# Kernel optimization log

Measured on AMD Instinct MI355X. Metric: run time of the kernel, lower is better.

## Reference

```python
import jax, jax.numpy as jnp
import numpy as np

HIDDEN = 768
HEADS = 12
HEAD_DIM = HIDDEN // HEADS
BETA = 0.5
BANDWIDTH = 1.0
D_INTRINSIC = 3
LN_EPS = 1e-12


def setup_inputs() -> dict:
    key = jax.random.key(0)
    ks = jax.random.split(key, 10)
    B, S, E = 2, 2048, HIDDEN
    sc = 1.0 / np.sqrt(E)
    return {
        "hidden_states": jax.random.normal(ks[0], (B, S, E), jnp.float32),
        "attention_mask": jnp.zeros((B, S), jnp.float32),
        "Wq": jax.random.normal(ks[1], (E, E), jnp.float32) * sc,
        "bq": jax.random.normal(ks[2], (E,), jnp.float32) * 0.02,
        "Wv": jax.random.normal(ks[3], (E, E), jnp.float32) * sc,
        "bv": jax.random.normal(ks[4], (E,), jnp.float32) * 0.02,
        "Wo": jax.random.normal(ks[5], (E, E), jnp.float32) * sc,
        "bo": jax.random.normal(ks[6], (E,), jnp.float32) * 0.02,
        "ln_g": jnp.ones((E,), jnp.float32),
        "ln_b": jnp.zeros((E,), jnp.float32),
    }


def _layernorm(x, g, b, eps=LN_EPS):
    mu = jnp.mean(x, axis=-1, keepdims=True)
    var = jnp.mean((x - mu) ** 2, axis=-1, keepdims=True)
    return (x - mu) * jax.lax.rsqrt(var + eps) * g + b


def reference(hidden_states, attention_mask, Wq, bq, Wv, bv, Wo, bo, ln_g, ln_b):
    B, S, E = hidden_states.shape
    H, D = HEADS, HEAD_DIM
    # projections (torch Linear: x @ W.T + b)
    q = (hidden_states @ Wq.T + bq).reshape(B, S, H, D).transpose(0, 2, 1, 3)  # [B,H,S,D]
    v = (hidden_states @ Wv.T + bv).reshape(B, S, H, D).transpose(0, 2, 1, 3)  # [B,H,S,D]
    # pairwise Euclidean distance (cdist) via norm expansion, safe sqrt
    qn = jnp.sum(q * q, axis=-1)  # [B,H,S]
    d2 = qn[:, :, :, None] + qn[:, :, None, :] - 2.0 * jnp.einsum("bhid,bhjd->bhij", q, q)
    dist = jnp.sqrt(jnp.maximum(d2, 1e-12))  # [B,H,S,S]
    # mask: positions with attention_mask < 0 get distance 2
    keep = (attention_mask >= 0)  # [B,S]
    pair_keep = keep[:, None, :, None] & keep[:, None, None, :]  # [B,1,S,S]
    dist = jnp.where(pair_keep, dist, 2.0)
    # power-law score + softmax
    attn_score = (1.0 + dist / (BANDWIDTH ** 0.5)) ** (-D_INTRINSIC - BETA)
    attn = jax.nn.softmax(attn_score, axis=-1)
    out = jnp.einsum("bhij,bhjd->bhid", attn, v)  # [B,H,S,D]
    out = out.transpose(0, 2, 1, 3).reshape(B, S, E)
    # ModelSelfOutput: dense + residual + LayerNorm (dropout=0, eval)
    out = out @ Wo.T + bo
    return _layernorm(out + hidden_states, ln_g, ln_b)
```

## Files before the change

kernel.cpp:

```cpp
#include <hip/hip_runtime.h>
#include <hip/hip_bf16.h>
#include <cstdint>
#include <cstddef>

#define S_LEN 2048
#define NH 12
#define HD 64
#define EDIM 768

typedef short bf16x8 __attribute__((ext_vector_type(8)));
typedef float f32x4  __attribute__((ext_vector_type(4)));

__device__ __forceinline__ unsigned short f2bf(float f) {
    return __bfloat16_as_ushort(__float2bfloat16(f));
}
__device__ __forceinline__ float bf2f(unsigned short u) {
    union { unsigned int i; float f; } x;
    x.i = ((unsigned int)u) << 16;
    return x.f;
}
__device__ __forceinline__ float rsq_f32(float x) {
#if __has_builtin(__builtin_amdgcn_rsqf)
    return __builtin_amdgcn_rsqf(x);
#else
    return __builtin_amdgcn_rcpf(__builtin_amdgcn_sqrtf(x));
#endif
}

__global__ __launch_bounds__(256) void precast_kernel(
    const float* __restrict__ hs, const float* __restrict__ Wq,
    const float* __restrict__ Wv, const float* __restrict__ Wo,
    unsigned short* __restrict__ hsb, unsigned short* __restrict__ Wqvb,
    unsigned short* __restrict__ Wob)
{
    const int i4 = blockIdx.x * 256 + threadIdx.x;
    const float* src;
    unsigned short* dst;
    int rel;
    if (i4 < 786432)        { src = hs; dst = hsb;            rel = i4; }
    else if (i4 < 933888)   { src = Wq; dst = Wqvb;           rel = i4 - 786432; }
    else if (i4 < 1081344)  { src = Wv; dst = Wqvb + 589824;  rel = i4 - 933888; }
    else                    { src = Wo; dst = Wob;            rel = i4 - 1081344; }
    float4 v = ((const float4*)src)[rel];
    ushort4 o;
    o.x = f2bf(v.x); o.y = f2bf(v.y); o.z = f2bf(v.z); o.w = f2bf(v.w);
    ((ushort4*)dst)[rel] = o;
}

__global__ __launch_bounds__(256) void qv_gemm(
    const unsigned short* __restrict__ hsb, const unsigned short* __restrict__ Wqvb,
    const float* __restrict__ bq, const float* __restrict__ bv,
    unsigned short* __restrict__ Qb, unsigned short* __restrict__ Vt,
    float* __restrict__ qn)
{
    __shared__ __align__(16) unsigned short As[64][40];
    __shared__ __align__(16) unsigned short Bs[128][40];

    const int t  = threadIdx.x;
    const int m0 = blockIdx.y << 6;
    const int c0 = blockIdx.x << 7;
    const bool isQ = (c0 < EDIM);
    const float* bias = isQ ? bq : bv;
    const int cb = isQ ? c0 : (c0 - EDIM);

    const int w  = t >> 6;
    const int l  = t & 63;
    const int ll = l & 15;
    const int lq = l >> 4;
    const int wx = w & 1;
    const int wy = w >> 1;

    const int srowA = t & 63;
    const int skA   = (t >> 6) << 3;
    const int srowB = t & 127;
    const int skB   = (t >> 7) << 4;

    f32x4 acc[2][4];
#pragma unroll
    for (int m = 0; m < 2; m++)
#pragma unroll
        for (int n = 0; n < 4; n++) acc[m][n] = (f32x4){0.f, 0.f, 0.f, 0.f};

    for (int k0 = 0; k0 < EDIM; k0 += 32) {
        bf16x8 va  = *(const bf16x8*)(hsb  + (size_t)(m0 + srowA) * EDIM + k0 + skA);
        bf16x8 vb0 = *(const bf16x8*)(Wqvb + (size_t)(c0 + srowB) * EDIM + k0 + skB);
        bf16x8 vb1 = *(const bf16x8*)(Wqvb + (size_t)(c0 + srowB) * EDIM + k0 + skB + 8);
        __syncthreads();
        *(bf16x8*)&As[srowA][skA]     = va;
        *(bf16x8*)&Bs[srowB][skB]     = vb0;
        *(bf16x8*)&Bs[srowB][skB + 8] = vb1;
        __syncthreads();
        bf16x8 aF[2], bF[4];
#pragma unroll
        for (int m = 0; m < 2; m++)
            aF[m] = *(const bf16x8*)&As[(wy << 5) + (m << 4) + ll][lq << 3];
#pragma unroll
        for (int n = 0; n < 4; n++)
            bF[n] = *(const bf16x8*)&Bs[(wx << 6) + (n << 4) + ll][lq << 3];
#pragma unroll
        for (int m = 0; m < 2; m++)
#pragma unroll
            for (int n = 0; n < 4; n++)
                acc[m][n] = __builtin_amdgcn_mfma_f32_16x16x32_bf16(aF[m], bF[n], acc[m][n], 0, 0, 0);
    }

    const int hcol0 = cb + (wx << 6);
    const int h = hcol0 >> 6;
    const int rowbase = m0 + (wy << 5);
    const int b = rowbase >> 11;
    const int sbase = rowbase & 2047;

    if (isQ) {
#pragma unroll
        for (int m = 0; m < 2; m++) {
#pragma unroll
            for (int r = 0; r < 4; r++) {
                const int si = sbase + (m << 4) + (lq << 2) + r;
                unsigned short* qrow = Qb + ((size_t)(b * NH + h) * S_LEN + si) * HD;
                float qsq = 0.f;
#pragma unroll
                for (int n = 0; n < 4; n++) {
                    unsigned short u = f2bf(acc[m][n][r] + bias[hcol0 + (n << 4) + ll]);
                    qrow[(n << 4) + ll] = u;
                    float f = bf2f(u);
                    qsq += f * f;
                }
                qsq += __shfl_xor(qsq, 1);
                qsq += __shfl_xor(qsq, 2);
                qsq += __shfl_xor(qsq, 4);
                qsq += __shfl_xor(qsq, 8);
                if (ll == 0) qn[(b * NH + h) * S_LEN + si] = qsq;
            }
        }
    } else {
#pragma unroll
        for (int m = 0; m < 2; m++) {
            const int si = sbase + (m << 4) + (lq << 2);
#pragma unroll
            for (int n = 0; n < 4; n++) {
                ushort4 o;
                o.x = f2bf(acc[m][n][0] + bias[hcol0 + (n << 4) + ll]);
                o.y = f2bf(acc[m][n][1] + bias[hcol0 + (n << 4) + ll]);
                o.z = f2bf(acc[m][n][2] + bias[hcol0 + (n << 4) + ll]);
                o.w = f2bf(acc[m][n][3] + bias[hcol0 + (n << 4) + ll]);
                *(ushort4*)&Vt[((size_t)(b * NH + h) * HD + (n << 4) + ll) * S_LEN + si] = o;
            }
        }
    }
}

template<int CUR>
__device__ __forceinline__ void attn_tile(
    int j0, int jn,
    const unsigned short* __restrict__ Qbase,
    const unsigned short* __restrict__ Vbase,
    const float* __restrict__ qnb, const float* __restrict__ mb,
    int ll, int lq,
    const bf16x8 (&aQ)[2][2],
    const float (&qni)[2][4], const float (&keepi)[2][4],
    const bf16x8& ones,
    f32x4 (&oacc)[2][4], f32x4 (&wacc)[2],
    bf16x8 (&nb0)[2], bf16x8 (&nb1)[2],
    bf16x8 (&vbuf)[2][4],
    unsigned short (&Wt)[2][2][16][40])
{
    constexpr int PRV = CUR ^ 1;
    __builtin_amdgcn_wave_barrier();
#pragma unroll
    for (int m = 0; m < 4; m++)
        vbuf[CUR][m] = *(const bf16x8*)(Vbase + (size_t)((m << 4) + ll) * S_LEN + j0 + (lq << 3));
    float qnjv[2], kjf[2];
#pragma unroll
    for (int n = 0; n < 2; n++) {
        int jc = j0 + (n << 4) + ll;
        qnjv[n] = qnb[jc];
        kjf[n]  = (mb[jc] >= 0.f) ? 1.f : 0.f;
    }
    f32x4 s[2][2];
#pragma unroll
    for (int s2 = 0; s2 < 2; s2++)
#pragma unroll
        for (int n = 0; n < 2; n++) {
            f32x4 c = (f32x4){0.f, 0.f, 0.f, 0.f};
            c = __builtin_amdgcn_mfma_f32_16x16x32_bf16(aQ[s2][0], nb0[n], c, 0, 0, 0);
            c = __builtin_amdgcn_mfma_f32_16x16x32_bf16(aQ[s2][1], nb1[n], c, 0, 0, 0);
            s[s2][n] = c;
        }
#pragma unroll
    for (int n = 0; n < 2; n++) {
        const unsigned short* bp = Qbase + (size_t)(jn + (n << 4) + ll) * HD + (lq << 3);
        nb0[n] = *(const bf16x8*)bp;
        nb1[n] = *(const bf16x8*)(bp + 32);
    }
#pragma unroll
    for (int s2 = 0; s2 < 2; s2++) {
        bf16x8 aP = *(const bf16x8*)&Wt[PRV][s2][ll][lq << 3];
#pragma unroll
        for (int m = 0; m < 4; m++)
            oacc[s2][m] = __builtin_amdgcn_mfma_f32_16x16x32_bf16(aP, vbuf[PRV][m], oacc[s2][m], 0, 0, 0);
        wacc[s2] = __builtin_amdgcn_mfma_f32_16x16x32_bf16(aP, ones, wacc[s2], 0, 0, 0);
    }
#pragma unroll
    for (int s2 = 0; s2 < 2; s2++)
#pragma unroll
        for (int n = 0; n < 2; n++)
#pragma unroll
            for (int r = 0; r < 4; r++) {
                float d2   = fmaf(-2.f, s[s2][n][r], qni[s2][r] + qnjv[n]);
                float dist = __builtin_amdgcn_sqrtf(fmaxf(d2, 1e-12f));
                dist = (keepi[s2][r] * kjf[n] != 0.f) ? dist : 2.0f;
                float x  = 1.0f + dist;
                float x2 = x * x;
                float x7 = x2 * x2 * x2 * x;
                float p  = rsq_f32(x7);
                float wv = fmaf(fmaf(fmaf(fmaf(0.041666668f, p, 0.16666667f),
                                          p, 0.5f), p, 1.0f), p, 1.0f);
                union { float f; unsigned int u; } cv; cv.f = wv;
                Wt[CUR][s2][(lq << 2) + r][(n << 4) + ll] =
                    (unsigned short)((cv.u + 0x8000u) >> 16);
            }
}

__global__ __launch_bounds__(256) void attn_kernel(
    const unsigned short* __restrict__ Qb, const unsigned short* __restrict__ Vt,
    const float* __restrict__ qn, const float* __restrict__ mask,
    unsigned short* __restrict__ AObf)
{
    __shared__ __align__(16) unsigned short Wt[4][2][2][16][40];

    const int t  = threadIdx.x;
    const int w  = t >> 6;
    const int l  = t & 63;
    const int ll = l & 15;
    const int lq = l >> 4;
    const int id = blockIdx.x;
    const int ib = id / 24;
    const int bh = id - ib * 24;
    const int b  = bh / NH;
    const int h  = bh - b * NH;
    const int iw = ib << 5;

    const unsigned short* Qbase = Qb + ((size_t)bh << 17);
    const unsigned short* Vbase = Vt + ((size_t)bh << 17);
    const float* qnb = qn + (bh << 11);
    const float* mb  = mask + (b << 11);

    unsigned short (&Wtw)[2][2][16][40] = Wt[w];

    const int tbase = w << 4;
    const int jb    = tbase << 5;

    bf16x8 aQ[2][2];
#pragma unroll
    for (int s2 = 0; s2 < 2; s2++) {
        const unsigned short* qp = Qbase + (size_t)(iw + (s2 << 4) + ll) * HD + (lq << 3);
        aQ[s2][0] = *(const bf16x8*)qp;
        aQ[s2][1] = *(const bf16x8*)(qp + 32);
    }

    float qni[2][4], keepi[2][4];
#pragma unroll
    for (int s2 = 0; s2 < 2; s2++)
#pragma unroll
        for (int r = 0; r < 4; r++) {
            int row = iw + (s2 << 4) + (lq << 2) + r;
            qni[s2][r]   = qnb[row];
            keepi[s2][r] = (mb[row] >= 0.f) ? 1.f : 0.f;
        }

    bf16x8 ones;
#pragma unroll
    for (int i = 0; i < 8; i++) ones[i] = (short)0x3F80;

    f32x4 oacc[2][4];
#pragma unroll
    for (int s2 = 0; s2 < 2; s2++)
#pragma unroll
        for (int m = 0; m < 4; m++) oacc[s2][m] = (f32x4){0.f, 0.f, 0.f, 0.f};
    f32x4 wacc[2];
    wacc[0] = (f32x4){0.f, 0.f, 0.f, 0.f};
    wacc[1] = (f32x4){0.f, 0.f, 0.f, 0.f};

    bf16x8 nb0[2], nb1[2];
#pragma unroll
    for (int n = 0; n < 2; n++) {
        const unsigned short* bp = Qbase + (size_t)(jb + (n << 4) + ll) * HD + (lq << 3);
        nb0[n] = *(const bf16x8*)bp;
        nb1[n] = *(const bf16x8*)(bp + 32);
    }
    bf16x8 vbuf[2][4];

    {
#pragma unroll
        for (int m = 0; m < 4; m++)
            vbuf[0][m] = *(const bf16x8*)(Vbase + (size_t)((m << 4) + ll) * S_LEN + jb + (lq << 3));
        float qnjv[2], kjf[2];
#pragma unroll
        for (int n = 0; n < 2; n++) {
            int jc = jb + (n << 4) + ll;
            qnjv[n] = qnb[jc];
            kjf[n]  = (mb[jc] >= 0.f) ? 1.f : 0.f;
        }
        f32x4 s[2][2];
#pragma unroll
        for (int s2 = 0; s2 < 2; s2++)
#pragma unroll
            for (int n = 0; n < 2; n++) {
                f32x4 c = (f32x4){0.f, 0.f, 0.f, 0.f};
                c = __builtin_amdgcn_mfma_f32_16x16x32_bf16(aQ[s2][0], nb0[n], c, 0, 0, 0);
                c = __builtin_amdgcn_mfma_f32_16x16x32_bf16(aQ[s2][1], nb1[n], c, 0, 0, 0);
                s[s2][n] = c;
            }
#pragma unroll
        for (int n = 0; n < 2; n++) {
            const unsigned short* bp = Qbase + (size_t)(jb + 32 + (n << 4) + ll) * HD + (lq << 3);
            nb0[n] = *(const bf16x8*)bp;
            nb1[n] = *(const bf16x8*)(bp + 32);
        }
#pragma unroll
        for (int s2 = 0; s2 < 2; s2++)
#pragma unroll
            for (int n = 0; n < 2; n++)
#pragma unroll
                for (int r = 0; r < 4; r++) {
                    float d2   = fmaf(-2.f, s[s2][n][r], qni[s2][r] + qnjv[n]);
                    float dist = __builtin_amdgcn_sqrtf(fmaxf(d2, 1e-12f));
                    dist = (keepi[s2][r] * kjf[n] != 0.f) ? dist : 2.0f;
                    float x  = 1.0f + dist;
                    float x2 = x * x;
                    float x7 = x2 * x2 * x2 * x;
                    float p  = rsq_f32(x7);
                    float wv = fmaf(fmaf(fmaf(fmaf(0.041666668f, p, 0.16666667f),
                                              p, 0.5f), p, 1.0f), p, 1.0f);
                    union { float f; unsigned int u; } cv; cv.f = wv;
                    Wtw[0][s2][(lq << 2) + r][(n << 4) + ll] =
                        (unsigned short)((cv.u + 0x8000u) >> 16);
                }
    }

    for (int tt = tbase + 1; tt <= tbase + 13; tt += 2) {
        attn_tile<1>(tt << 5, (tt + 1) << 5, Qbase, Vbase, qnb, mb, ll, lq,
                     aQ, qni, keepi, ones, oacc, wacc, nb0, nb1, vbuf, Wtw);
        attn_tile<0>((tt + 1) << 5, (tt + 2) << 5, Qbase, Vbase, qnb, mb, ll, lq,
                     aQ, qni, keepi, ones, oacc, wacc, nb0, nb1, vbuf, Wtw);
    }
    attn_tile<1>((tbase + 15) << 5, 0, Qbase, Vbase, qnb, mb, ll, lq,
                 aQ, qni, keepi, ones, oacc, wacc, nb0, nb1, vbuf, Wtw);

    __builtin_amdgcn_wave_barrier();
#pragma unroll
    for (int s2 = 0; s2 < 2; s2++) {
        bf16x8 aP = *(const bf16x8*)&Wtw[1][s2][ll][lq << 3];
#pragma unroll
        for (int m = 0; m < 4; m++)
            oacc[s2][m] = __builtin_amdgcn_mfma_f32_16x16x32_bf16(aP, vbuf[1][m], oacc[s2][m], 0, 0, 0);
        wacc[s2] = __builtin_amdgcn_mfma_f32_16x16x32_bf16(aP, ones, wacc[s2], 0, 0, 0);
    }

    float* red = (float*)Wt;
    __syncthreads();
    if (w >= 2) {
        float* p = red + (((w - 2) << 6) + l);
#pragma unroll
        for (int s2 = 0; s2 < 2; s2++)
#pragma unroll
            for (int m = 0; m < 4; m++)
#pragma unroll
                for (int r = 0; r < 4; r++)
                    p[((((s2 << 2) + m) << 2) + r) * 128] = oacc[s2][m][r];
#pragma unroll
        for (int s2 = 0; s2 < 2; s2++)
#pragma unroll
            for (int r = 0; r < 4; r++)
                p[(32 + (s2 << 2) + r) * 128] = wacc[s2][r];
    }
    __syncthreads();
    if (w < 2) {
        float* p = red + ((w << 6) + l);
#pragma unroll
        for (int s2 = 0; s2 < 2; s2++)
#pragma unroll
            for (int m = 0; m < 4; m++)
#pragma unroll
                for (int r = 0; r < 4; r++)
                    oacc[s2][m][r] += p[((((s2 << 2) + m) << 2) + r) * 128];
#pragma unroll
        for (int s2 = 0; s2 < 2; s2++)
#pragma unroll
            for (int r = 0; r < 4; r++)
                wacc[s2][r] += p[(32 + (s2 << 2) + r) * 128];
    }
    __syncthreads();
    if (w == 1) {
        float* p = red + l;
#pragma unroll
        for (int s2 = 0; s2 < 2; s2++)
#pragma unroll
            for (int m = 0; m < 4; m++)
#pragma unroll
                for (int r = 0; r < 4; r++)
                    p[((((s2 << 2) + m) << 2) + r) * 128] = oacc[s2][m][r];
#pragma unroll
        for (int s2 = 0; s2 < 2; s2++)
#pragma unroll
            for (int r = 0; r < 4; r++)
                p[(32 + (s2 << 2) + r) * 128] = wacc[s2][r];
    }
    __syncthreads();
    if (w == 0) {
        float* p = red + l;
#pragma unroll
        for (int s2 = 0; s2 < 2; s2++)
#pragma unroll
            for (int m = 0; m < 4; m++)
#pragma unroll
                for (int r = 0; r < 4; r++)
                    oacc[s2][m][r] += p[((((s2 << 2) + m) << 2) + r) * 128];
#pragma unroll
        for (int s2 = 0; s2 < 2; s2++)
#pragma unroll
            for (int r = 0; r < 4; r++)
                wacc[s2][r] += p[(32 + (s2 << 2) + r) * 128];

#pragma unroll
        for (int s2 = 0; s2 < 2; s2++)
#pragma unroll
            for (int r = 0; r < 4; r++) {
                float inv = 1.0f / wacc[s2][r];
                const int row = iw + (s2 << 4) + (lq << 2) + r;
                unsigned short* dst = AObf + (size_t)((b << 11) + row) * EDIM + (h << 6);
#pragma unroll
                for (int m = 0; m < 4; m++)
                    dst[(m << 4) + ll] = f2bf(oacc[s2][m][r] * inv);
            }
    }
}

__global__ __launch_bounds__(256) void oproj_gemm(
    const unsigned short* __restrict__ AObf, const unsigned short* __restrict__ Wob,
    const float* __restrict__ bo, const float* __restrict__ hs,
    float* __restrict__ TMP)
{
    __shared__ __align__(16) unsigned short As[64][40];
    __shared__ __align__(16) unsigned short Bs[64][40];

    const int t  = threadIdx.x;
    const int m0 = blockIdx.y << 6;
    const int c0 = blockIdx.x << 6;

    const int w  = t >> 6;
    const int l  = t & 63;
    const int ll = l & 15;
    const int lq = l >> 4;
    const int wx = w & 1;
    const int wy = w >> 1;

    const int srow = t & 63;
    const int sk   = (t >> 6) << 3;

    f32x4 acc[2][2];
#pragma unroll
    for (int m = 0; m < 2; m++)
#pragma unroll
        for (int n = 0; n < 2; n++) acc[m][n] = (f32x4){0.f, 0.f, 0.f, 0.f};

    for (int k0 = 0; k0 < EDIM; k0 += 32) {
        bf16x8 va = *(const bf16x8*)(AObf + (size_t)(m0 + srow) * EDIM + k0 + sk);
        bf16x8 vb = *(const bf16x8*)(Wob  + (size_t)(c0 + srow) * EDIM + k0 + sk);
        __syncthreads();
        *(bf16x8*)&As[srow][sk] = va;
        *(bf16x8*)&Bs[srow][sk] = vb;
        __syncthreads();
        bf16x8 aF[2], bF[2];
#pragma unroll
        for (int m = 0; m < 2; m++)
            aF[m] = *(const bf16x8*)&As[(wy << 5) + (m << 4) + ll][lq << 3];
#pragma unroll
        for (int n = 0; n < 2; n++)
            bF[n] = *(const bf16x8*)&Bs[(wx << 5) + (n << 4) + ll][lq << 3];
#pragma unroll
        for (int m = 0; m < 2; m++)
#pragma unroll
            for (int n = 0; n < 2; n++)
                acc[m][n] = __builtin_amdgcn_mfma_f32_16x16x32_bf16(aF[m], bF[n], acc[m][n], 0, 0, 0);
    }

#pragma unroll
    for (int m = 0; m < 2; m++) {
#pragma unroll
        for (int r = 0; r < 4; r++) {
            const int row = m0 + (wy << 5) + (m << 4) + (lq << 2) + r;
#pragma unroll
            for (int n = 0; n < 2; n++) {
                const int col = c0 + (wx << 5) + (n << 4) + ll;
                TMP[(size_t)row * EDIM + col] =
                    acc[m][n][r] + bo[col] + hs[(size_t)row * EDIM + col];
            }
        }
    }
}

__global__ __launch_bounds__(256) void ln_kernel(
    const float* __restrict__ X, const float* __restrict__ g,
    const float* __restrict__ be, float* __restrict__ out)
{
    const int row = blockIdx.x;
    const int t = threadIdx.x;
    const float* x = X + (size_t)row * EDIM;

    float s = 0.f, sq = 0.f;
#pragma unroll
    for (int c = t; c < EDIM; c += 256) {
        float v = x[c];
        s += v; sq += v * v;
    }
#pragma unroll
    for (int m = 1; m < 64; m <<= 1) {
        s  += __shfl_xor(s, m);
        sq += __shfl_xor(sq, m);
    }
    __shared__ float ss[4], ssq[4];
    const int w = t >> 6;
    if ((t & 63) == 0) { ss[w] = s; ssq[w] = sq; }
    __syncthreads();
    s  = ss[0] + ss[1] + ss[2] + ss[3];
    sq = ssq[0] + ssq[1] + ssq[2] + ssq[3];
    const float mu  = s * (1.f / EDIM);
    const float var = sq * (1.f / EDIM) - mu * mu;
    const float rstd = 1.0f / sqrtf(var + 1e-12f);

#pragma unroll
    for (int c = t; c < EDIM; c += 256) {
        out[(size_t)row * EDIM + c] = (x[c] - mu) * rstd * g[c] + be[c];
    }
}

extern "C" void kernel_launch(void* const* d_in, const int* in_sizes, int n_in,
                              void* d_out, int out_size, void* d_ws, size_t ws_size,
                              hipStream_t stream) {
    const float* hs   = (const float*)d_in[0];
    const float* mask = (const float*)d_in[1];
    const float* Wq   = (const float*)d_in[2];
    const float* bq   = (const float*)d_in[3];
    const float* Wv   = (const float*)d_in[4];
    const float* bv   = (const float*)d_in[5];
    const float* Wo   = (const float*)d_in[6];
    const float* bo   = (const float*)d_in[7];
    const float* g    = (const float*)d_in[8];
    const float* be   = (const float*)d_in[9];

    char* w8 = (char*)d_ws;
    unsigned short* Qb   = (unsigned short*)(w8);
    unsigned short* Vt   = (unsigned short*)(w8 +  6291456);
    float*          qn   = (float*)        (w8 + 12582912);
    unsigned short* AObf = (unsigned short*)(w8 + 12779520);
    unsigned short* hsb  = (unsigned short*)(w8 + 19070976);
    unsigned short* Wqvb = (unsigned short*)(w8 + 25362432);
    unsigned short* Wob  = (unsigned short*)(w8 + 27721728);
    float*          TMP  = (float*)(w8);

    precast_kernel<<<dim3(4800),    256, 0, stream>>>(hs, Wq, Wv, Wo, hsb, Wqvb, Wob);
    qv_gemm       <<<dim3(12, 64),  256, 0, stream>>>(hsb, Wqvb, bq, bv, Qb, Vt, qn);
    attn_kernel   <<<dim3(1536),    256, 0, stream>>>(Qb, Vt, qn, mask, AObf);
    oproj_gemm    <<<dim3(12, 64),  256, 0, stream>>>(AObf, Wob, bo, hs, TMP);
    ln_kernel     <<<dim3(4096),    256, 0, stream>>>(TMP, g, be, (float*)d_out);
}
```

Measured before the change: 254.0 us.

## Use two waves per attention block with packed f32x2 score math

Each attention block now runs 2 waves instead of 4, and each wave covers 32 key tiles instead of 16. This halves the cross-wave reduction to a single shared-memory exchange stage and halves the LDS footprint. The elementwise score computation is rewritten with f32x2 vector ops so it can map to packed FMA and multiply. The key-norm and mask loads are prefetched one tile ahead, and the mask select is folded into an FMA. The trade-off is fewer waves per block and longer per-wave loops, which lowers latency hiding within a block, though more blocks can be resident at once.

```diff
diff --git a/kernel.cpp b/kernel.cpp
--- a/kernel.cpp
+++ b/kernel.cpp
@@ -10,6 +10,7 @@
 
 typedef short bf16x8 __attribute__((ext_vector_type(8)));
 typedef float f32x4  __attribute__((ext_vector_type(4)));
+typedef float f32x2  __attribute__((ext_vector_type(2)));
 
 __device__ __forceinline__ unsigned short f2bf(float f) {
     return __bfloat16_as_ushort(__float2bfloat16(f));
@@ -150,18 +151,19 @@
 }
 
 template<int CUR>
-__device__ __forceinline__ void attn_tile(
+__device__ __forceinline__ void attn_tile32(
     int j0, int jn,
     const unsigned short* __restrict__ Qbase,
     const unsigned short* __restrict__ Vbase,
     const float* __restrict__ qnb, const float* __restrict__ mb,
     int ll, int lq,
     const bf16x8 (&aQ)[2][2],
-    const float (&qni)[2][4], const float (&keepi)[2][4],
+    const f32x2 (&qni2)[2][2], const f32x2 (&keepi2)[2][2],
     const bf16x8& ones,
     f32x4 (&oacc)[2][4], f32x4 (&wacc)[2],
     bf16x8 (&nb0)[2], bf16x8 (&nb1)[2],
     bf16x8 (&vbuf)[2][4],
+    float (&qnjv)[2][2], float (&kjm)[2][2],
     unsigned short (&Wt)[2][2][16][40])
 {
     constexpr int PRV = CUR ^ 1;
@@ -169,13 +171,6 @@
 #pragma unroll
     for (int m = 0; m < 4; m++)
         vbuf[CUR][m] = *(const bf16x8*)(Vbase + (size_t)((m << 4) + ll) * S_LEN + j0 + (lq << 3));
-    float qnjv[2], kjf[2];
-#pragma unroll
-    for (int n = 0; n < 2; n++) {
-        int jc = j0 + (n << 4) + ll;
-        qnjv[n] = qnb[jc];
-        kjf[n]  = (mb[jc] >= 0.f) ? 1.f : 0.f;
-    }
     f32x4 s[2][2];
 #pragma unroll
     for (int s2 = 0; s2 < 2; s2++)
@@ -191,6 +186,9 @@
         const unsigned short* bp = Qbase + (size_t)(jn + (n << 4) + ll) * HD + (lq << 3);
         nb0[n] = *(const bf16x8*)bp;
         nb1[n] = *(const bf16x8*)(bp + 32);
+        int jc = jn + (n << 4) + ll;
+        qnjv[PRV][n] = qnb[jc];
+        kjm[PRV][n]  = (mb[jc] >= 0.f) ? 1.f : 0.f;
     }
 #pragma unroll
     for (int s2 = 0; s2 < 2; s2++) {
@@ -203,30 +201,43 @@
 #pragma unroll
     for (int s2 = 0; s2 < 2; s2++)
 #pragma unroll
-        for (int n = 0; n < 2; n++)
-#pragma unroll
-            for (int r = 0; r < 4; r++) {
-                float d2   = fmaf(-2.f, s[s2][n][r], qni[s2][r] + qnjv[n]);
-                float dist = __builtin_amdgcn_sqrtf(fmaxf(d2, 1e-12f));
-                dist = (keepi[s2][r] * kjf[n] != 0.f) ? dist : 2.0f;
-                float x  = 1.0f + dist;
-                float x2 = x * x;
-                float x7 = x2 * x2 * x2 * x;
-                float p  = rsq_f32(x7);
-                float wv = fmaf(fmaf(fmaf(fmaf(0.041666668f, p, 0.16666667f),
-                                          p, 0.5f), p, 1.0f), p, 1.0f);
-                union { float f; unsigned int u; } cv; cv.f = wv;
-                Wt[CUR][s2][(lq << 2) + r][(n << 4) + ll] =
-                    (unsigned short)((cv.u + 0x8000u) >> 16);
-            }
-}
-
-__global__ __launch_bounds__(256) void attn_kernel(
+        for (int n = 0; n < 2; n++) {
+            const f32x2 qv = (f32x2)(qnjv[CUR][n]);
+            const f32x2 kj = (f32x2)(kjm[CUR][n]);
+#pragma unroll
+            for (int pr = 0; pr < 2; pr++) {
+                f32x2 sp = { s[s2][n][2*pr], s[s2][n][2*pr + 1] };
+                f32x2 d2 = __builtin_elementwise_fma(sp, (f32x2)(-2.f), qni2[s2][pr] + qv);
+                d2 = __builtin_elementwise_max(d2, (f32x2)(1e-12f));
+                f32x2 dist = { __builtin_amdgcn_sqrtf(d2.x), __builtin_amdgcn_sqrtf(d2.y) };
+                f32x2 km = keepi2[s2][pr] * kj;
+                f32x2 x  = __builtin_elementwise_fma(km, dist + (f32x2)(-2.f), (f32x2)(3.f));
+                f32x2 x2 = x * x;
+                f32x2 x4 = x2 * x2;
+                f32x2 x6 = x4 * x2;
+                f32x2 x7 = x6 * x;
+                f32x2 p  = { rsq_f32(x7.x), rsq_f32(x7.y) };
+                f32x2 wv = __builtin_elementwise_fma(
+                    __builtin_elementwise_fma(
+                        __builtin_elementwise_fma(
+                            __builtin_elementwise_fma((f32x2)(0.041666668f), p, (f32x2)(0.16666667f)),
+                            p, (f32x2)(0.5f)),
+                        p, (f32x2)(1.0f)),
+                    p, (f32x2)(1.0f));
+                union { float f; unsigned int u; } c0, c1;
+                c0.f = wv.x; c1.f = wv.y;
+                Wt[CUR][s2][(lq << 2) + 2*pr    ][(n << 4) + ll] = (unsigned short)((c0.u + 0x8000u) >> 16);
+                Wt[CUR][s2][(lq << 2) + 2*pr + 1][(n << 4) + ll] = (unsigned short)((c1.u + 0x8000u) >> 16);
+            }
+        }
+}
+
+__global__ __launch_bounds__(128) void attn_kernel(
     const unsigned short* __restrict__ Qb, const unsigned short* __restrict__ Vt,
     const float* __restrict__ qn, const float* __restrict__ mask,
     unsigned short* __restrict__ AObf)
 {
-    __shared__ __align__(16) unsigned short Wt[4][2][2][16][40];
+    __shared__ __align__(16) unsigned short Wt[2][2][2][16][40];
 
     const int t  = threadIdx.x;
     const int w  = t >> 6;
@@ -247,7 +258,7 @@
 
     unsigned short (&Wtw)[2][2][16][40] = Wt[w];
 
-    const int tbase = w << 4;
+    const int tbase = w << 5;
     const int jb    = tbase << 5;
 
     bf16x8 aQ[2][2];
@@ -258,14 +269,15 @@
         aQ[s2][1] = *(const bf16x8*)(qp + 32);
     }
 
-    float qni[2][4], keepi[2][4];
+    f32x2 qni2[2][2], keepi2[2][2];
 #pragma unroll
     for (int s2 = 0; s2 < 2; s2++)
 #pragma unroll
-        for (int r = 0; r < 4; r++) {
-            int row = iw + (s2 << 4) + (lq << 2) + r;
-            qni[s2][r]   = qnb[row];
-            keepi[s2][r] = (mb[row] >= 0.f) ? 1.f : 0.f;
+        for (int pr = 0; pr < 2; pr++) {
+            int r0 = iw + (s2 << 4) + (lq << 2) + 2*pr;
+            qni2[s2][pr]   = (f32x2){ qnb[r0], qnb[r0 + 1] };
+            keepi2[s2][pr] = (f32x2){ (mb[r0] >= 0.f) ? 1.f : 0.f,
+                                      (mb[r0 + 1] >= 0.f) ? 1.f : 0.f };
         }
 
     bf16x8 ones;
@@ -282,11 +294,15 @@
     wacc[1] = (f32x4){0.f, 0.f, 0.f, 0.f};
 
     bf16x8 nb0[2], nb1[2];
+    float qnjv[2][2], kjm[2][2];
 #pragma unroll
     for (int n = 0; n < 2; n++) {
         const unsigned short* bp = Qbase + (size_t)(jb + (n << 4) + ll) * HD + (lq << 3);
         nb0[n] = *(const bf16x8*)bp;
         nb1[n] = *(const bf16x8*)(bp + 32);
+        int jc = jb + (n << 4) + ll;
+        qnjv[0][n] = qnb[jc];
+        kjm[0][n]  = (mb[jc] >= 0.f) ? 1.f : 0.f;
     }
     bf16x8 vbuf[2][4];
 
@@ -294,13 +310,6 @@
 #pragma unroll
         for (int m = 0; m < 4; m++)
             vbuf[0][m] = *(const bf16x8*)(Vbase + (size_t)((m << 4) + ll) * S_LEN + jb + (lq << 3));
-        float qnjv[2], kjf[2];
-#pragma unroll
-        for (int n = 0; n < 2; n++) {
-            int jc = jb + (n << 4) + ll;
-            qnjv[n] = qnb[jc];
-            kjf[n]  = (mb[jc] >= 0.f) ? 1.f : 0.f;
-        }
         f32x4 s[2][2];
 #pragma unroll
         for (int s2 = 0; s2 < 2; s2++)
@@ -316,36 +325,52 @@
             const unsigned short* bp = Qbase + (size_t)(jb + 32 + (n << 4) + ll) * HD + (lq << 3);
             nb0[n] = *(const bf16x8*)bp;
             nb1[n] = *(const bf16x8*)(bp + 32);
-        }
-#pragma unroll
-        for (int s2 = 0; s2 < 2; s2++)
-#pragma unroll
-            for (int n = 0; n < 2; n++)
-#pragma unroll
-                for (int r = 0; r < 4; r++) {
-                    float d2   = fmaf(-2.f, s[s2][n][r], qni[s2][r] + qnjv[n]);
-                    float dist = __builtin_amdgcn_sqrtf(fmaxf(d2, 1e-12f));
-                    dist = (keepi[s2][r] * kjf[n] != 0.f) ? dist : 2.0f;
-                    float x  = 1.0f + dist;
-                    float x2 = x * x;
-                    float x7 = x2 * x2 * x2 * x;
-                    float p  = rsq_f32(x7);
-                    float wv = fmaf(fmaf(fmaf(fmaf(0.041666668f, p, 0.16666667f),
-                                              p, 0.5f), p, 1.0f), p, 1.0f);
-                    union { float f; unsigned int u; } cv; cv.f = wv;
-                    Wtw[0][s2][(lq << 2) + r][(n << 4) + ll] =
-                        (unsigned short)((cv.u + 0x8000u) >> 16);
+            int jc = jb + 32 + (n << 4) + ll;
+            qnjv[1][n] = qnb[jc];
+            kjm[1][n]  = (mb[jc] >= 0.f) ? 1.f : 0.f;
+        }
+#pragma unroll
+        for (int s2 = 0; s2 < 2; s2++)
+#pragma unroll
+            for (int n = 0; n < 2; n++) {
+                const f32x2 qv = (f32x2)(qnjv[0][n]);
+                const f32x2 kj = (f32x2)(kjm[0][n]);
+#pragma unroll
+                for (int pr = 0; pr < 2; pr++) {
+                    f32x2 sp = { s[s2][n][2*pr], s[s2][n][2*pr + 1] };
+                    f32x2 d2 = __builtin_elementwise_fma(sp, (f32x2)(-2.f), qni2[s2][pr] + qv);
+                    d2 = __builtin_elementwise_max(d2, (f32x2)(1e-12f));
+                    f32x2 dist = { __builtin_amdgcn_sqrtf(d2.x), __builtin_amdgcn_sqrtf(d2.y) };
+                    f32x2 km = keepi2[s2][pr] * kj;
+                    f32x2 x  = __builtin_elementwise_fma(km, dist + (f32x2)(-2.f), (f32x2)(3.f));
+                    f32x2 x2 = x * x;
+                    f32x2 x4 = x2 * x2;
+                    f32x2 x6 = x4 * x2;
+                    f32x2 x7 = x6 * x;
+                    f32x2 p  = { rsq_f32(x7.x), rsq_f32(x7.y) };
+                    f32x2 wv = __builtin_elementwise_fma(
+                        __builtin_elementwise_fma(
+                            __builtin_elementwise_fma(
+                                __builtin_elementwise_fma((f32x2)(0.041666668f), p, (f32x2)(0.16666667f)),
+                                p, (f32x2)(0.5f)),
+                            p, (f32x2)(1.0f)),
+                        p, (f32x2)(1.0f));
+                    union { float f; unsigned int u; } c0, c1;
+                    c0.f = wv.x; c1.f = wv.y;
+                    Wtw[0][s2][(lq << 2) + 2*pr    ][(n << 4) + ll] = (unsigned short)((c0.u + 0x8000u) >> 16);
+                    Wtw[0][s2][(lq << 2) + 2*pr + 1][(n << 4) + ll] = (unsigned short)((c1.u + 0x8000u) >> 16);
                 }
-    }
-
-    for (int tt = tbase + 1; tt <= tbase + 13; tt += 2) {
-        attn_tile<1>(tt << 5, (tt + 1) << 5, Qbase, Vbase, qnb, mb, ll, lq,
-                     aQ, qni, keepi, ones, oacc, wacc, nb0, nb1, vbuf, Wtw);
-        attn_tile<0>((tt + 1) << 5, (tt + 2) << 5, Qbase, Vbase, qnb, mb, ll, lq,
-                     aQ, qni, keepi, ones, oacc, wacc, nb0, nb1, vbuf, Wtw);
-    }
-    attn_tile<1>((tbase + 15) << 5, 0, Qbase, Vbase, qnb, mb, ll, lq,
-                 aQ, qni, keepi, ones, oacc, wacc, nb0, nb1, vbuf, Wtw);
+            }
+    }
+
+    for (int tt = tbase + 1; tt <= tbase + 29; tt += 2) {
+        attn_tile32<1>(tt << 5, (tt + 1) << 5, Qbase, Vbase, qnb, mb, ll, lq,
+                       aQ, qni2, keepi2, ones, oacc, wacc, nb0, nb1, vbuf, qnjv, kjm, Wtw);
+        attn_tile32<0>((tt + 1) << 5, (tt + 2) << 5, Qbase, Vbase, qnb, mb, ll, lq,
+                       aQ, qni2, keepi2, ones, oacc, wacc, nb0, nb1, vbuf, qnjv, kjm, Wtw);
+    }
+    attn_tile32<1>((tbase + 31) << 5, 0, Qbase, Vbase, qnb, mb, ll, lq,
+                   aQ, qni2, keepi2, ones, oacc, wacc, nb0, nb1, vbuf, qnjv, kjm, Wtw);
 
     __builtin_amdgcn_wave_barrier();
 #pragma unroll
@@ -359,38 +384,6 @@
 
     float* red = (float*)Wt;
     __syncthreads();
-    if (w >= 2) {
-        float* p = red + (((w - 2) << 6) + l);
-#pragma unroll
-        for (int s2 = 0; s2 < 2; s2++)
-#pragma unroll
-            for (int m = 0; m < 4; m++)
-#pragma unroll
-                for (int r = 0; r < 4; r++)
-                    p[((((s2 << 2) + m) << 2) + r) * 128] = oacc[s2][m][r];
-#pragma unroll
-        for (int s2 = 0; s2 < 2; s2++)
-#pragma unroll
-            for (int r = 0; r < 4; r++)
-                p[(32 + (s2 << 2) + r) * 128] = wacc[s2][r];
-    }
-    __syncthreads();
-    if (w < 2) {
-        float* p = red + ((w << 6) + l);
-#pragma unroll
-        for (int s2 = 0; s2 < 2; s2++)
-#pragma unroll
-            for (int m = 0; m < 4; m++)
-#pragma unroll
-                for (int r = 0; r < 4; r++)
-                    oacc[s2][m][r] += p[((((s2 << 2) + m) << 2) + r) * 128];
-#pragma unroll
-        for (int s2 = 0; s2 < 2; s2++)
-#pragma unroll
-            for (int r = 0; r < 4; r++)
-                wacc[s2][r] += p[(32 + (s2 << 2) + r) * 128];
-    }
-    __syncthreads();
     if (w == 1) {
         float* p = red + l;
 #pragma unroll
@@ -399,12 +392,12 @@
             for (int m = 0; m < 4; m++)
 #pragma unroll
                 for (int r = 0; r < 4; r++)
-                    p[((((s2 << 2) + m) << 2) + r) * 128] = oacc[s2][m][r];
+                    p[((((s2 << 2) + m) << 2) + r) << 6] = oacc[s2][m][r];
 #pragma unroll
         for (int s2 = 0; s2 < 2; s2++)
 #pragma unroll
             for (int r = 0; r < 4; r++)
-                p[(32 + (s2 << 2) + r) * 128] = wacc[s2][r];
+                p[(32 + (s2 << 2) + r) << 6] = wacc[s2][r];
     }
     __syncthreads();
     if (w == 0) {
@@ -415,12 +408,12 @@
             for (int m = 0; m < 4; m++)
 #pragma unroll
                 for (int r = 0; r < 4; r++)
-                    oacc[s2][m][r] += p[((((s2 << 2) + m) << 2) + r) * 128];
+                    oacc[s2][m][r] += p[((((s2 << 2) + m) << 2) + r) << 6];
 #pragma unroll
         for (int s2 = 0; s2 < 2; s2++)
 #pragma unroll
             for (int r = 0; r < 4; r++)
-                wacc[s2][r] += p[(32 + (s2 << 2) + r) * 128];
+                wacc[s2][r] += p[(32 + (s2 << 2) + r) << 6];
 
 #pragma unroll
         for (int s2 = 0; s2 < 2; s2++)
@@ -561,7 +554,7 @@
 
     precast_kernel<<<dim3(4800),    256, 0, stream>>>(hs, Wq, Wv, Wo, hsb, Wqvb, Wob);
     qv_gemm       <<<dim3(12, 64),  256, 0, stream>>>(hsb, Wqvb, bq, bv, Qb, Vt, qn);
-    attn_kernel   <<<dim3(1536),    256, 0, stream>>>(Qb, Vt, qn, mask, AObf);
+    attn_kernel   <<<dim3(1536),    128, 0, stream>>>(Qb, Vt, qn, mask, AObf);
     oproj_gemm    <<<dim3(12, 64),  256, 0, stream>>>(AObf, Wob, bo, hs, TMP);
     ln_kernel     <<<dim3(4096),    256, 0, stream>>>(TMP, g, be, (float*)d_out);
 }
```

After: 264.1 us. +4.0%, slower.
